# Performance work log

Measured on AMD Instinct MI355X. Metric: run time of the kernel, lower is better.

The kernel has to match this reference:

```python
import jax, jax.numpy as jnp
import numpy as np

NEG_SLOPE = 0.2  # DGL GATConv default leaky_relu slope


def gat_conv(x, src, dst, W, attn_l, attn_r, bias, res_W):
    """DGL GATConv (eval mode, residual=True with linear res_fc, bias).
    x: [N, F_in]; src/dst: [E]; W: [F_in, H*D]; attn_l/r: [H, D];
    bias: [H*D]; res_W: [F_in, H*D]. Returns [N, H, D]."""
    N = x.shape[0]
    H, D = attn_l.shape
    feat = (x @ W).reshape(N, H, D)
    el = jnp.sum(feat * attn_l, axis=-1)  # [N, H]
    er = jnp.sum(feat * attn_r, axis=-1)  # [N, H]
    e = jax.nn.leaky_relu(el[src] + er[dst], NEG_SLOPE)  # [E, H]
    # edge softmax over incoming edges of each dst node (numerically stable)
    m = jnp.full((N, H), -jnp.inf, dtype=e.dtype).at[dst].max(e)
    ex = jnp.exp(e - m[dst])
    s = jnp.zeros((N, H), dtype=e.dtype).at[dst].add(ex)
    alpha = ex / s[dst]  # [E, H]
    # scatter-aggregate messages alpha * feat[src] into dst
    rst = jnp.zeros((N, H, D), dtype=x.dtype).at[dst].add(alpha[:, :, None] * feat[src])
    rst = rst + (x @ res_W).reshape(N, H, D) + bias.reshape(1, H, D)
    return rst


def setup_inputs() -> dict:
    key = jax.random.key(0)
    N, E, F_IN, HID, OUT, H = 20000, 320000, 128, 128, 128, 4
    ks = jax.random.split(key, 32)
    ki = iter(range(32))

    def rn(shape, scale=0.05):
        return jax.random.normal(ks[next(ki)], shape, dtype=jnp.float32) * scale

    inp = {
        "n_feat": jax.random.normal(ks[next(ki)], (N, F_IN), dtype=jnp.float32),
        "src": jax.random.randint(ks[next(ki)], (E,), 0, N, dtype=jnp.int32),
        "dst": jax.random.randint(ks[next(ki)], (E,), 0, N, dtype=jnp.int32),
        # input GATConv: F_IN -> H x HID
        "W0": rn((F_IN, H * HID)), "al0": rn((H, HID)), "ar0": rn((H, HID)),
        "b0": rn((H * HID,)), "rW0": rn((F_IN, H * HID)),
        "DW0": rn((H * HID, HID)), "Db0": rn((HID,)),
        # middle GATConv: HID -> H x HID
        "W1": rn((HID, H * HID)), "al1": rn((H, HID)), "ar1": rn((H, HID)),
        "b1": rn((H * HID,)), "rW1": rn((HID, H * HID)),
        "DW1": rn((H * HID, HID)), "Db1": rn((HID,)),
        # output GATConv: HID -> H x OUT
        "W2": rn((HID, H * OUT)), "al2": rn((H, OUT)), "ar2": rn((H, OUT)),
        "b2": rn((H * OUT,)), "rW2": rn((HID, H * OUT)),
    }
    return inp


def reference(n_feat, src, dst,
              W0, al0, ar0, b0, rW0, DW0, Db0,
              W1, al1, ar1, b1, rW1, DW1, Db1,
              W2, al2, ar2, b2, rW2):
    N = n_feat.shape[0]
    relu = jax.nn.relu
    # input GAT block
    h = relu(gat_conv(n_feat, src, dst, W0, al0, ar0, b0, rW0))  # [N, H, HID]
    h = relu(h.reshape(N, -1) @ DW0 + Db0)                        # [N, HID]
    # middle GAT block
    h = relu(gat_conv(h, src, dst, W1, al1, ar1, b1, rW1))
    h = relu(h.reshape(N, -1) @ DW1 + Db1)
    # output GAT + head-mean + graph max pooling (single graph)
    h = relu(gat_conv(h, src, dst, W2, al2, ar2, b2, rW2))        # [N, H, OUT]
    h = relu(jnp.mean(h, axis=-2))                                 # [N, OUT]
    return jnp.max(h, axis=0, keepdims=True)                       # [1, OUT]
```

## Files before the change

### kernel.cpp

```cpp
#include <hip/hip_runtime.h>
#include <hip/hip_bf16.h>


typedef __attribute__((ext_vector_type(8))) short bf16x8;
typedef __attribute__((ext_vector_type(4))) float f32x4;
typedef __hip_bfloat16 bf16_t;

__device__ __forceinline__ unsigned int pack_bf16(float lo, float hi) {
  return (((unsigned int)__bfloat16_as_ushort(__float2bfloat16(hi))) << 16) |
         (unsigned int)__bfloat16_as_ushort(__float2bfloat16(lo));
}

__device__ __forceinline__ void gload_lds16(const void* g, void* l) {
  __builtin_amdgcn_global_load_lds(
      (const __attribute__((address_space(1))) void*)g,
      (__attribute__((address_space(3))) void*)l, 16, 0, 0);
}

__global__ __launch_bounds__(256) void mega_prep(
    const float* __restrict__ W0, const float* __restrict__ rW0,
    const float* __restrict__ W1, const float* __restrict__ rW1,
    const float* __restrict__ W2, const float* __restrict__ rW2,
    const float* __restrict__ DW0, const float* __restrict__ DW1,
    const float* __restrict__ al0, const float* __restrict__ ar0,
    const float* __restrict__ al1, const float* __restrict__ ar1,
    const float* __restrict__ al2, const float* __restrict__ ar2,
    const float* __restrict__ n_feat, bf16_t* __restrict__ wts,
    float* __restrict__ ALR, bf16_t* __restrict__ xbf,
    int* __restrict__ counts, float* __restrict__ partials, int N) {
  __shared__ float tile[32][33];
  int b = blockIdx.x, tid = threadIdx.x;
  int r = tid >> 5, c = tid & 31;

  if (b < 384) {
    int mat = b >> 6;
    int t = b & 63;
    int kt = t >> 4, nt = t & 15;
    int L = mat >> 1, isR = mat & 1;
    const float* S = (L == 0) ? (isR ? rW0 : W0)
                   : (L == 1) ? (isR ? rW1 : W1) : (isR ? rW2 : W2);
    bf16_t* D = wts + L * 131072 + isR * 65536;
#pragma unroll
    for (int rr = 0; rr < 4; rr++)
      tile[r + rr * 8][c] = S[(kt * 32 + r + rr * 8) * 512 + nt * 32 + c];
    __syncthreads();
#pragma unroll
    for (int rr = 0; rr < 4; rr++)
      D[(nt * 32 + r + rr * 8) * 128 + kt * 32 + c] =
          __float2bfloat16(tile[c][r + rr * 8]);
  } else if (b < 512) {
    int i = b - 384;
    int mat = i >> 6;
    int t = i & 63;
    int kt = t & 15, nt = t >> 4;
    const float* S = mat ? DW1 : DW0;
    bf16_t* D = wts + 393216 + mat * 65536;
#pragma unroll
    for (int rr = 0; rr < 4; rr++)
      tile[r + rr * 8][c] = S[(kt * 32 + r + rr * 8) * 128 + nt * 32 + c];
    __syncthreads();
#pragma unroll
    for (int rr = 0; rr < 4; rr++)
      D[(nt * 32 + r + rr * 8) * 512 + kt * 32 + c] =
          __float2bfloat16(tile[c][r + rr * 8]);
  } else if (b < 524) {
    int idx = (b - 512) * 256 + tid;
    if (idx < 3072) {
      int L = idx >> 10;
      int k = (idx >> 3) & 127;
      int cc = idx & 7;
      int h = cc & 3;
      const float* W = (L == 0) ? W0 : (L == 1) ? W1 : W2;
      const float* a = (cc < 4) ? ((L == 0) ? al0 : (L == 1) ? al1 : al2)
                                : ((L == 0) ? ar0 : (L == 1) ? ar1 : ar2);
      float s = 0.f;
      for (int d = 0; d < 128; d++) s += W[k * 512 + h * 128 + d] * a[h * 128 + d];
      ALR[idx] = s;
    }
  } else if (b < 3024) {
    int i = ((b - 524) * 256 + tid) * 4;
    if (i < N * 128) {
      float4 v = *(const float4*)(n_feat + i);
      xbf[i + 0] = __float2bfloat16(v.x);
      xbf[i + 1] = __float2bfloat16(v.y);
      xbf[i + 2] = __float2bfloat16(v.z);
      xbf[i + 3] = __float2bfloat16(v.w);
    }
  } else {
    for (int i = tid; i < N; i += 256) counts[i] = 0;
    for (int i = tid; i < 64 * 128; i += 256) partials[i] = 0.f;
  }
}

template <bool COUNT>
__global__ __launch_bounds__(256) void gemm128el(
    const bf16_t* __restrict__ A, const bf16_t* __restrict__ Bt,
    const float* __restrict__ ALRl, bf16_t* __restrict__ C,
    float* __restrict__ el, float* __restrict__ er, int M, int ldc, int K,
    const int* __restrict__ dst, int* __restrict__ counts, int E) {
  __shared__ bf16_t As[128 * 64];
  __shared__ bf16_t Bs[128 * 64];
  int tid = threadIdx.x;
  int rowBase = blockIdx.y * 128;

  if (COUNT && blockIdx.x == 9) {
    int stride = gridDim.y * 256;
    for (int i = blockIdx.y * 256 + tid; i < E; i += stride)
      atomicAdd(&counts[dst[i]], 1);
    return;
  }

  if (blockIdx.x == 8) {
    float* sALR = (float*)As;
#pragma unroll
    for (int j = 0; j < 4; j++) sALR[tid * 4 + j] = ALRl[tid * 4 + j];
    __syncthreads();
    int row = rowBase + (tid >> 1);
    int half = tid & 1;
    if (row < M) {
      const bf16_t* xr = A + (size_t)row * K + half * 64;
      float s[8] = {};
#pragma unroll
      for (int g = 0; g < 8; g++) {
        bf16x8 v = *(const bf16x8*)(xr + g * 8);
#pragma unroll
        for (int e = 0; e < 8; e++) {
          float f = __uint_as_float(((unsigned int)(unsigned short)v[e]) << 16);
          const float* Ak = sALR + (half * 64 + g * 8 + e) * 8;
#pragma unroll
          for (int cc = 0; cc < 8; cc++) s[cc] += f * Ak[cc];
        }
      }
#pragma unroll
      for (int cc = 0; cc < 8; cc++) s[cc] += __shfl_xor(s[cc], 1);
      if (half == 0)
        *(float4*)(el + row * 4) = make_float4(s[0], s[1], s[2], s[3]);
      else
        *(float4*)(er + row * 4) = make_float4(s[4], s[5], s[6], s[7]);
    }
    return;
  }

  int lane = tid & 63, wave = tid >> 6;
  int q = lane >> 4, r16 = lane & 15;
  int wm = (wave >> 1) * 64, wn = (wave & 1) * 64;
  int colBase = blockIdx.x * 128;

  f32x4 acc[4][4] = {};

  for (int k0 = 0; k0 < K; k0 += 64) {
#pragma unroll
    for (int p = 0; p < 4; p++) {
      int slotb = (wave * 4 + p) * 64;
      int s = slotb + lane;
      int r = s >> 3;
      int c = (s & 7) ^ (r & 7);
      int gr = rowBase + r;
      if (gr > M - 1) gr = M - 1;
      gload_lds16(A + (size_t)gr * K + k0 + c * 8, (char*)As + (size_t)slotb * 16);
      gload_lds16(Bt + (size_t)(colBase + r) * K + k0 + c * 8,
                  (char*)Bs + (size_t)slotb * 16);
    }
    __syncthreads();
#pragma unroll
    for (int ks = 0; ks < 64; ks += 32) {
      int koff = ks >> 3;
      bf16x8 af[4], bfr[4];
#pragma unroll
      for (int i = 0; i < 4; i++) {
        int R = wm + i * 16 + r16;
        int slot = R * 8 + ((q + koff) ^ (R & 7));
        af[i] = *(const bf16x8*)((const char*)As + (size_t)slot * 16);
      }
#pragma unroll
      for (int j = 0; j < 4; j++) {
        int R = wn + j * 16 + r16;
        int slot = R * 8 + ((q + koff) ^ (R & 7));
        bfr[j] = *(const bf16x8*)((const char*)Bs + (size_t)slot * 16);
      }
#pragma unroll
      for (int i = 0; i < 4; i++)
#pragma unroll
        for (int j = 0; j < 4; j++)
          acc[i][j] = __builtin_amdgcn_mfma_f32_16x16x32_bf16(af[i], bfr[j], acc[i][j], 0, 0, 0);
    }
    __syncthreads();
  }

  int odd = lane & 1;
  int colb0 = r16 & ~1;
#pragma unroll
  for (int i = 0; i < 4; i++) {
#pragma unroll
    for (int r = 0; r < 4; r++) {
      int row = rowBase + wm + i * 16 + q * 4 + r;
#pragma unroll
      for (int jp = 0; jp < 2; jp++) {
        float a0 = acc[i][2 * jp][r];
        float a1 = acc[i][2 * jp + 1][r];
        float p0 = __shfl_xor(a0, 1);
        float p1 = __shfl_xor(a1, 1);
        float lo = odd ? p1 : a0;
        float hi = odd ? a1 : p0;
        int col = colBase + wn + (2 * jp + odd) * 16 + colb0;
        if (row < M)
          *(unsigned int*)(C + (size_t)row * ldc + col) = pack_bf16(lo, hi);
      }
    }
  }
}

__global__ __launch_bounds__(256) void mfma_gemm64(
    const bf16_t* __restrict__ A, const bf16_t* __restrict__ Bt,
    const float* __restrict__ bias, bf16_t* __restrict__ C,
    int M, int ldc, int K) {
  __shared__ bf16_t As[64 * 64];
  __shared__ bf16_t Bs[64 * 64];
  int tid = threadIdx.x;
  int lane = tid & 63, wave = tid >> 6;
  int q = lane >> 4, r16 = lane & 15;
  int wm = (wave >> 1) * 32, wn = (wave & 1) * 32;
  int rowBase = blockIdx.y * 64, colBase = blockIdx.x * 64;

  f32x4 acc[2][2] = {};

  for (int k0 = 0; k0 < K; k0 += 64) {
#pragma unroll
    for (int p = 0; p < 2; p++) {
      int slotb = (wave * 2 + p) * 64;
      int s = slotb + lane;
      int r = s >> 3;
      int c = (s & 7) ^ (r & 7);
      int gr = rowBase + r;
      if (gr > M - 1) gr = M - 1;
      gload_lds16(A + (size_t)gr * K + k0 + c * 8, (char*)As + (size_t)slotb * 16);
      gload_lds16(Bt + (size_t)(colBase + r) * K + k0 + c * 8,
                  (char*)Bs + (size_t)slotb * 16);
    }
    __syncthreads();
#pragma unroll
    for (int ks = 0; ks < 64; ks += 32) {
      int koff = ks >> 3;
      bf16x8 af[2], bfr[2];
#pragma unroll
      for (int i = 0; i < 2; i++) {
        int R = wm + i * 16 + r16;
        int slot = R * 8 + ((q + koff) ^ (R & 7));
        af[i] = *(const bf16x8*)((const char*)As + (size_t)slot * 16);
      }
#pragma unroll
      for (int j = 0; j < 2; j++) {
        int R = wn + j * 16 + r16;
        int slot = R * 8 + ((q + koff) ^ (R & 7));
        bfr[j] = *(const bf16x8*)((const char*)Bs + (size_t)slot * 16);
      }
#pragma unroll
      for (int i = 0; i < 2; i++)
#pragma unroll
        for (int j = 0; j < 2; j++)
          acc[i][j] = __builtin_amdgcn_mfma_f32_16x16x32_bf16(af[i], bfr[j], acc[i][j], 0, 0, 0);
    }
    __syncthreads();
  }

  int odd = lane & 1;
  int colb0 = r16 & ~1;
#pragma unroll
  for (int i = 0; i < 2; i++) {
#pragma unroll
    for (int r = 0; r < 4; r++) {
      int row = rowBase + wm + i * 16 + q * 4 + r;
      float a0 = acc[i][0][r];
      float a1 = acc[i][1][r];
      float p0 = __shfl_xor(a0, 1);
      float p1 = __shfl_xor(a1, 1);
      float lo = odd ? p1 : a0;
      float hi = odd ? a1 : p0;
      int col = colBase + wn + odd * 16 + colb0;
      if (row < M) {
        float o0 = fmaxf(lo + bias[col], 0.f);
        float o1 = fmaxf(hi + bias[col + 1], 0.f);
        *(unsigned int*)(C + (size_t)row * ldc + col) = pack_bf16(o0, o1);
      }
    }
  }
}

__global__ __launch_bounds__(1024) void scan_kernel(const int* __restrict__ counts,
                                                    int* __restrict__ row_ptr,
                                                    int* __restrict__ cursor, int N) {
  __shared__ int sums[1024];
  int t = threadIdx.x;
  int chunk = (N + 1023) / 1024;
  int begin = t * chunk;
  int end = begin + chunk;
  if (end > N) end = N;
  int s = 0;
  for (int i = begin; i < end; i++) s += counts[i];
  sums[t] = s;
  __syncthreads();
  for (int off = 1; off < 1024; off <<= 1) {
    int v = (t >= off) ? sums[t - off] : 0;
    __syncthreads();
    sums[t] += v;
    __syncthreads();
  }
  int run = (t == 0) ? 0 : sums[t - 1];
  for (int i = begin; i < end; i++) {
    row_ptr[i] = run;
    cursor[i] = run;
    run += counts[i];
  }
  if (t == 1023) row_ptr[N] = sums[1023];
}

__global__ __launch_bounds__(256) void scatter_kernel(
    const int* __restrict__ src, const int* __restrict__ dst,
    int* __restrict__ cursor, int* __restrict__ edge_src, int E) {
  int i = blockIdx.x * blockDim.x + threadIdx.x;
  if (i < E) {
    int d = dst[i];
    int pos = atomicAdd(&cursor[d], 1);
    edge_src[pos] = src[i];
  }
}

template <bool POOL>
__global__ __launch_bounds__(256) void gat_agg_kernel(
    const bf16_t* __restrict__ fused,
    const float* __restrict__ el, const float* __restrict__ er,
    const float* __restrict__ bias, const int* __restrict__ row_ptr,
    const int* __restrict__ edge_src, bf16_t* __restrict__ out,
    float* __restrict__ partials, int N) {
  __shared__ float accL[4][64][8];
  __shared__ float ssumL[4][4];
  int n = blockIdx.x;
  int tid = threadIdx.x;
  int wave = tid >> 6, lane = tid & 63;
  int hh = lane >> 4;
  int start = row_ptr[n];
  int deg = row_ptr[n + 1] - start;
  float er_h = er[n * 4 + hh];

  float acc[8] = {};
  float ssum = 0.f;
  const bf16_t* fbase = fused + (size_t)lane * 8;
  for (int i = wave; i < deg; i += 4) {
    int s = edge_src[start + i];
    float e = el[s * 4 + hh] + er_h;
    e = (e > 0.f) ? e : 0.2f * e;
    float w = __expf(e);
    ssum += w;
    uint4 f = *(const uint4*)(fbase + (size_t)s * 1024);
    unsigned int u[4] = {f.x, f.y, f.z, f.w};
#pragma unroll
    for (int j = 0; j < 4; j++) {
      acc[2 * j] += w * __uint_as_float(u[j] << 16);
      acc[2 * j + 1] += w * __uint_as_float(u[j] & 0xffff0000u);
    }
  }
  *(float4*)&accL[wave][lane][0] = make_float4(acc[0], acc[1], acc[2], acc[3]);
  *(float4*)&accL[wave][lane][4] = make_float4(acc[4], acc[5], acc[6], acc[7]);
  if ((lane & 15) == 0) ssumL[wave][hh] = ssum;
  __syncthreads();

  int d = tid * 2;
  int l = d >> 3, j = d & 7;
  float a0 = 0.f, a1 = 0.f;
#pragma unroll
  for (int w = 0; w < 4; w++) {
    a0 += accL[w][l][j];
    a1 += accL[w][l][j + 1];
  }
  int h = tid >> 6;
  float ssum4 = ssumL[0][h] + ssumL[1][h] + ssumL[2][h] + ssumL[3][h];
  float inv = (deg > 0) ? 1.f / ssum4 : 0.f;
  unsigned int ru = *(const unsigned int*)(fused + (size_t)n * 1024 + 512 + d);
  float2 bv = *(const float2*)(bias + d);
  float o0 = fmaxf(a0 * inv + __uint_as_float(ru << 16) + bv.x, 0.f);
  float o1 = fmaxf(a1 * inv + __uint_as_float(ru & 0xffff0000u) + bv.y, 0.f);

  if (!POOL) {
    *(unsigned int*)(out + (size_t)n * 512 + d) = pack_bf16(o0, o1);
  } else {
    float2* red = (float2*)accL;
    __syncthreads();
    red[tid] = make_float2(o0, o1);
    __syncthreads();
    if (tid < 64) {
      float m0 = 0.25f * (red[tid].x + red[tid + 64].x + red[tid + 128].x + red[tid + 192].x);
      float m1 = 0.25f * (red[tid].y + red[tid + 64].y + red[tid + 128].y + red[tid + 192].y);
      float* slot = partials + (n & 63) * 128;
      atomicMax((int*)slot + 2 * tid, __float_as_int(m0));
      atomicMax((int*)slot + 2 * tid + 1, __float_as_int(m1));
    }
  }
}

__global__ __launch_bounds__(128) void pool_finish(const float* __restrict__ partials,
                                                   float* __restrict__ out) {
  int d = threadIdx.x;
  float m = 0.f;
#pragma unroll 8
  for (int s = 0; s < 64; s++) m = fmaxf(m, partials[s * 128 + d]);
  out[d] = m;
}

extern "C" void kernel_launch(void* const* d_in, const int* in_sizes, int n_in,
                              void* d_out, int out_size, void* d_ws, size_t ws_size,
                              hipStream_t stream) {
  const float* n_feat = (const float*)d_in[0];
  const int* src = (const int*)d_in[1];
  const int* dst = (const int*)d_in[2];
  const float* W0 = (const float*)d_in[3];
  const float* al0 = (const float*)d_in[4];
  const float* ar0 = (const float*)d_in[5];
  const float* b0 = (const float*)d_in[6];
  const float* rW0 = (const float*)d_in[7];
  const float* DW0 = (const float*)d_in[8];
  const float* Db0 = (const float*)d_in[9];
  const float* W1 = (const float*)d_in[10];
  const float* al1 = (const float*)d_in[11];
  const float* ar1 = (const float*)d_in[12];
  const float* b1 = (const float*)d_in[13];
  const float* rW1 = (const float*)d_in[14];
  const float* DW1 = (const float*)d_in[15];
  const float* Db1 = (const float*)d_in[16];
  const float* W2 = (const float*)d_in[17];
  const float* al2 = (const float*)d_in[18];
  const float* ar2 = (const float*)d_in[19];
  const float* b2 = (const float*)d_in[20];
  const float* rW2 = (const float*)d_in[21];

  const int N = in_sizes[0] / 128;
  const int E = in_sizes[1];

  bf16_t* xbf = (bf16_t*)d_ws;
  bf16_t* fusedFR = xbf + (size_t)N * 128;
  bf16_t* outC = fusedFR + (size_t)N * 1024;
  bf16_t* denseD = outC + (size_t)N * 512;
  bf16_t* wts = denseD + (size_t)N * 128;
  float* ALR = (float*)(wts + 524288);
  float* el = ALR + 3072;
  float* er = el + (size_t)N * 4;
  float* partials = er + (size_t)N * 4;
  int* counts = (int*)(partials + 64 * 128);
  int* row_ptr = counts + N;
  int* cursor = row_ptr + (N + 1);
  int* edge_src = cursor + N;

  bf16_t* FW0 = wts;
  bf16_t* FW1 = wts + 131072;
  bf16_t* FW2 = wts + 262144;
  bf16_t* DWt0 = wts + 393216;
  bf16_t* DWt1 = wts + 458752;

  mega_prep<<<3025, 256, 0, stream>>>(
      W0, rW0, W1, rW1, W2, rW2, DW0, DW1,
      al0, ar0, al1, ar1, al2, ar2,
      n_feat, wts, ALR, xbf, counts, partials, N);

  int nRow = (N + 127) / 128;
  dim3 gF0(10, nRow);
  dim3 gF(9, nRow);
  dim3 gD(2, (N + 63) / 64);

  gemm128el<true><<<gF0, 256, 0, stream>>>(xbf, FW0, ALR, fusedFR, el, er,
                                           N, 1024, 128, dst, counts, E);
  scan_kernel<<<1, 1024, 0, stream>>>(counts, row_ptr, cursor, N);
  scatter_kernel<<<(E + 255) / 256, 256, 0, stream>>>(src, dst, cursor, edge_src, E);

  gat_agg_kernel<false><<<N, 256, 0, stream>>>(fusedFR, el, er, b0, row_ptr,
                                               edge_src, outC, nullptr, N);
  mfma_gemm64<<<gD, 256, 0, stream>>>(outC, DWt0, Db0, denseD, N, 128, 512);
  gemm128el<false><<<gF, 256, 0, stream>>>(denseD, FW1, ALR + 1024, fusedFR,
                                           el, er, N, 1024, 128, nullptr, nullptr, 0);
  gat_agg_kernel<false><<<N, 256, 0, stream>>>(fusedFR, el, er, b1, row_ptr,
                                               edge_src, outC, nullptr, N);
  mfma_gemm64<<<gD, 256, 0, stream>>>(outC, DWt1, Db1, denseD, N, 128, 512);
  gemm128el<false><<<gF, 256, 0, stream>>>(denseD, FW2, ALR + 2048, fusedFR,
                                           el, er, N, 1024, 128, nullptr, nullptr, 0);
  gat_agg_kernel<true><<<N, 256, 0, stream>>>(fusedFR, el, er, b2, row_ptr,
                                              edge_src, nullptr, partials, N);
  pool_finish<<<1, 128, 0, stream>>>(partials, (float*)d_out);
}
```

Before: 413.5 us.

## Precompute per-edge attention weights in CSR order and split feat/res buffers

Attention weights exp(leaky_relu(el[src]+er[dst])) are now computed once per edge in a separate pass, stored contiguously in CSR order, and read by the aggregation kernel instead of being gathered from el and recomputed there. The GEMM output is also split into separate feature and residual buffers with row stride 512, so the feature gathers in aggregation touch a denser array. In exchange it adds two extra kernel launches plus writing and reading an E*4 float weight array and an edge_dst array.

```diff
diff --git a/kernel.cpp b/kernel.cpp
--- a/kernel.cpp
+++ b/kernel.cpp
@@ -6,9 +6,16 @@
 typedef __attribute__((ext_vector_type(4))) float f32x4;
 typedef __hip_bfloat16 bf16_t;
 
+#define NEG_SLOPE 0.2f
+
 __device__ __forceinline__ unsigned int pack_bf16(float lo, float hi) {
   return (((unsigned int)__bfloat16_as_ushort(__float2bfloat16(hi))) << 16) |
          (unsigned int)__bfloat16_as_ushort(__float2bfloat16(lo));
+}
+
+__device__ __forceinline__ float leaky_exp(float e) {
+  e = (e > 0.f) ? e : NEG_SLOPE * e;
+  return __expf(e);
 }
 
 __device__ __forceinline__ void gload_lds16(const void* g, void* l) {
@@ -95,8 +102,9 @@
 template <bool COUNT>
 __global__ __launch_bounds__(256) void gemm128el(
     const bf16_t* __restrict__ A, const bf16_t* __restrict__ Bt,
-    const float* __restrict__ ALRl, bf16_t* __restrict__ C,
-    float* __restrict__ el, float* __restrict__ er, int M, int ldc, int K,
+    const float* __restrict__ ALRl, bf16_t* __restrict__ featB,
+    bf16_t* __restrict__ resB,
+    float* __restrict__ el, float* __restrict__ er, int M, int K,
     const int* __restrict__ dst, int* __restrict__ counts, int E) {
   __shared__ bf16_t As[128 * 64];
   __shared__ bf16_t Bs[128 * 64];
@@ -145,6 +153,8 @@
   int q = lane >> 4, r16 = lane & 15;
   int wm = (wave >> 1) * 64, wn = (wave & 1) * 64;
   int colBase = blockIdx.x * 128;
+  bf16_t* Cb = (colBase < 512) ? featB : resB;
+  int colOff = (colBase < 512) ? colBase : colBase - 512;
 
   f32x4 acc[4][4] = {};
 
@@ -202,9 +212,9 @@
         float p1 = __shfl_xor(a1, 1);
         float lo = odd ? p1 : a0;
         float hi = odd ? a1 : p0;
-        int col = colBase + wn + (2 * jp + odd) * 16 + colb0;
+        int col = colOff + wn + (2 * jp + odd) * 16 + colb0;
         if (row < M)
-          *(unsigned int*)(C + (size_t)row * ldc + col) = pack_bf16(lo, hi);
+          *(unsigned int*)(Cb + (size_t)row * 512 + col) = pack_bf16(lo, hi);
       }
     }
   }
@@ -314,21 +324,53 @@
   if (t == 1023) row_ptr[N] = sums[1023];
 }
 
-__global__ __launch_bounds__(256) void scatter_kernel(
+__global__ __launch_bounds__(256) void scatter_w_kernel(
     const int* __restrict__ src, const int* __restrict__ dst,
-    int* __restrict__ cursor, int* __restrict__ edge_src, int E) {
+    int* __restrict__ cursor, int* __restrict__ edge_src,
+    int* __restrict__ edge_dst, const float* __restrict__ el,
+    const float* __restrict__ er, float* __restrict__ wcsr, int E) {
   int i = blockIdx.x * blockDim.x + threadIdx.x;
   if (i < E) {
+    int s = src[i];
     int d = dst[i];
     int pos = atomicAdd(&cursor[d], 1);
-    edge_src[pos] = src[i];
+    edge_src[pos] = s;
+    edge_dst[pos] = d;
+    float4 elv = *(const float4*)(el + s * 4);
+    float4 erv = *(const float4*)(er + d * 4);
+    float4 w;
+    w.x = leaky_exp(elv.x + erv.x);
+    w.y = leaky_exp(elv.y + erv.y);
+    w.z = leaky_exp(elv.z + erv.z);
+    w.w = leaky_exp(elv.w + erv.w);
+    *(float4*)(wcsr + (size_t)pos * 4) = w;
+  }
+}
+
+__global__ __launch_bounds__(256) void w_pass_kernel(
+    const int* __restrict__ edge_src, const int* __restrict__ edge_dst,
+    const float* __restrict__ el, const float* __restrict__ er,
+    float* __restrict__ wcsr, int E) {
+  int p = blockIdx.x * blockDim.x + threadIdx.x;
+  if (p < E) {
+    int s = edge_src[p];
+    int d = edge_dst[p];
+    float4 elv = *(const float4*)(el + s * 4);
+    float4 erv = *(const float4*)(er + d * 4);
+    float4 w;
+    w.x = leaky_exp(elv.x + erv.x);
+    w.y = leaky_exp(elv.y + erv.y);
+    w.z = leaky_exp(elv.z + erv.z);
+    w.w = leaky_exp(elv.w + erv.w);
+    *(float4*)(wcsr + (size_t)p * 4) = w;
   }
 }
 
 template <bool POOL>
 __global__ __launch_bounds__(256) void gat_agg_kernel(
-    const bf16_t* __restrict__ fused,
-    const float* __restrict__ el, const float* __restrict__ er,
+    const bf16_t* __restrict__ featB,
+    const bf16_t* __restrict__ resB,
+    const float* __restrict__ wcsr,
     const float* __restrict__ bias, const int* __restrict__ row_ptr,
     const int* __restrict__ edge_src, bf16_t* __restrict__ out,
     float* __restrict__ partials, int N) {
@@ -340,23 +382,21 @@
   int hh = lane >> 4;
   int start = row_ptr[n];
   int deg = row_ptr[n + 1] - start;
-  float er_h = er[n * 4 + hh];
 
   float acc[8] = {};
   float ssum = 0.f;
-  const bf16_t* fbase = fused + (size_t)lane * 8;
+  const bf16_t* fbase = featB + (size_t)lane * 8;
   for (int i = wave; i < deg; i += 4) {
-    int s = edge_src[start + i];
-    float e = el[s * 4 + hh] + er_h;
-    e = (e > 0.f) ? e : 0.2f * e;
-    float w = __expf(e);
-    ssum += w;
-    uint4 f = *(const uint4*)(fbase + (size_t)s * 1024);
+    int p = start + i;
+    int s = edge_src[p];
+    float wv = wcsr[(size_t)p * 4 + hh];
+    ssum += wv;
+    uint4 f = *(const uint4*)(fbase + (size_t)s * 512);
     unsigned int u[4] = {f.x, f.y, f.z, f.w};
 #pragma unroll
     for (int j = 0; j < 4; j++) {
-      acc[2 * j] += w * __uint_as_float(u[j] << 16);
-      acc[2 * j + 1] += w * __uint_as_float(u[j] & 0xffff0000u);
+      acc[2 * j] += wv * __uint_as_float(u[j] << 16);
+      acc[2 * j + 1] += wv * __uint_as_float(u[j] & 0xffff0000u);
     }
   }
   *(float4*)&accL[wave][lane][0] = make_float4(acc[0], acc[1], acc[2], acc[3]);
@@ -375,7 +415,7 @@
   int h = tid >> 6;
   float ssum4 = ssumL[0][h] + ssumL[1][h] + ssumL[2][h] + ssumL[3][h];
   float inv = (deg > 0) ? 1.f / ssum4 : 0.f;
-  unsigned int ru = *(const unsigned int*)(fused + (size_t)n * 1024 + 512 + d);
+  unsigned int ru = *(const unsigned int*)(resB + (size_t)n * 512 + d);
   float2 bv = *(const float2*)(bias + d);
   float o0 = fmaxf(a0 * inv + __uint_as_float(ru << 16) + bv.x, 0.f);
   float o1 = fmaxf(a1 * inv + __uint_as_float(ru & 0xffff0000u) + bv.y, 0.f);
@@ -436,18 +476,21 @@
   const int E = in_sizes[1];
 
   bf16_t* xbf = (bf16_t*)d_ws;
-  bf16_t* fusedFR = xbf + (size_t)N * 128;
-  bf16_t* outC = fusedFR + (size_t)N * 1024;
+  bf16_t* featB = xbf + (size_t)N * 128;
+  bf16_t* resB = featB + (size_t)N * 512;
+  bf16_t* outC = resB + (size_t)N * 512;
   bf16_t* denseD = outC + (size_t)N * 512;
   bf16_t* wts = denseD + (size_t)N * 128;
   float* ALR = (float*)(wts + 524288);
   float* el = ALR + 3072;
   float* er = el + (size_t)N * 4;
   float* partials = er + (size_t)N * 4;
-  int* counts = (int*)(partials + 64 * 128);
+  float* wcsr = partials + 64 * 128;
+  int* counts = (int*)(wcsr + (size_t)E * 4);
   int* row_ptr = counts + N;
   int* cursor = row_ptr + (N + 1);
   int* edge_src = cursor + N;
+  int* edge_dst = edge_src + E;
 
   bf16_t* FW0 = wts;
   bf16_t* FW1 = wts + 131072;
@@ -464,23 +507,27 @@
   dim3 gF0(10, nRow);
   dim3 gF(9, nRow);
   dim3 gD(2, (N + 63) / 64);
-
-  gemm128el<true><<<gF0, 256, 0, stream>>>(xbf, FW0, ALR, fusedFR, el, er,
-                                           N, 1024, 128, dst, counts, E);
+  int gE = (E + 255) / 256;
+
+  gemm128el<true><<<gF0, 256, 0, stream>>>(xbf, FW0, ALR, featB, resB, el, er,
+                                           N, 128, dst, counts, E);
   scan_kernel<<<1, 1024, 0, stream>>>(counts, row_ptr, cursor, N);
-  scatter_kernel<<<(E + 255) / 256, 256, 0, stream>>>(src, dst, cursor, edge_src, E);
-
-  gat_agg_kernel<false><<<N, 256, 0, stream>>>(fusedFR, el, er, b0, row_ptr,
+  scatter_w_kernel<<<gE, 256, 0, stream>>>(src, dst, cursor, edge_src, edge_dst,
+                                           el, er, wcsr, E);
+
+  gat_agg_kernel<false><<<N, 256, 0, stream>>>(featB, resB, wcsr, b0, row_ptr,
                                                edge_src, outC, nullptr, N);
   mfma_gemm64<<<gD, 256, 0, stream>>>(outC, DWt0, Db0, denseD, N, 128, 512);
-  gemm128el<false><<<gF, 256, 0, stream>>>(denseD, FW1, ALR + 1024, fusedFR,
-                                           el, er, N, 1024, 128, nullptr, nullptr, 0);
-  gat_agg_kernel<false><<<N, 256, 0, stream>>>(fusedFR, el, er, b1, row_ptr,
+  gemm128el<false><<<gF, 256, 0, stream>>>(denseD, FW1, ALR + 1024, featB, resB,
+                                           el, er, N, 128, nullptr, nullptr, 0);
+  w_pass_kernel<<<gE, 256, 0, stream>>>(edge_src, edge_dst, el, er, wcsr, E);
+  gat_agg_kernel<false><<<N, 256, 0, stream>>>(featB, resB, wcsr, b1, row_ptr,
                                                edge_src, outC, nullptr, N);
   mfma_gemm64<<<gD, 256, 0, stream>>>(outC, DWt1, Db1, denseD, N, 128, 512);
-  gemm128el<false><<<gF, 256, 0, stream>>>(denseD, FW2, ALR + 2048, fusedFR,
-                                           el, er, N, 1024, 128, nullptr, nullptr, 0);
-  gat_agg_kernel<true><<<N, 256, 0, stream>>>(fusedFR, el, er, b2, row_ptr,
+  gemm128el<false><<<gF, 256, 0, stream>>>(denseD, FW2, ALR + 2048, featB, resB,
+                                           el, er, N, 128, nullptr, nullptr, 0);
+  w_pass_kernel<<<gE, 256, 0, stream>>>(edge_src, edge_dst, el, er, wcsr, E);
+  gat_agg_kernel<true><<<N, 256, 0, stream>>>(featB, resB, wcsr, b2, row_ptr,
                                               edge_src, nullptr, partials, N);
   pool_finish<<<1, 128, 0, stream>>>(partials, (float*)d_out);
 }
```

Result: slower. 424.1 us (+2.6%).
